# Performance work log

Measured on AMD Instinct MI355X. Metric: run time of the kernel, lower is better.

## Reference

```python
import jax, jax.numpy as jnp
import numpy as np

DIM = 256
NUM_HEADS = 4
HEAD_DIM = DIM // NUM_HEADS
EPS = 1e-5


def setup_inputs() -> dict:
    key = jax.random.key(0)
    ks = jax.random.split(key, 8)
    B, N, C = 8, 2048, DIM
    s = 0.02
    return {
        "x": jax.random.normal(ks[0], (B, N, C), jnp.float32),
        "qkv_w": jax.random.normal(ks[1], (C, 3 * C), jnp.float32) * s,
        "qkv_b": jnp.zeros((3 * C,), jnp.float32),
        "proj_w": jax.random.normal(ks[2], (C, C), jnp.float32) * s,
        "proj_b": jnp.zeros((C,), jnp.float32),
        "ln1_g": jnp.ones((C,), jnp.float32),
        "ln1_b": jnp.zeros((C,), jnp.float32),
        "ln2_g": jnp.ones((C,), jnp.float32),
        "ln2_b": jnp.zeros((C,), jnp.float32),
        "mlp_w1": jax.random.normal(ks[3], (C, 2 * C), jnp.float32) * s,
        "mlp_b1": jnp.zeros((2 * C,), jnp.float32),
        "mlp_w2": jax.random.normal(ks[4], (2 * C, C), jnp.float32) * s,
        "mlp_b2": jnp.zeros((C,), jnp.float32),
    }


def _layernorm(x, g, b):
    mu = jnp.mean(x, axis=-1, keepdims=True)
    var = jnp.mean(jnp.square(x - mu), axis=-1, keepdims=True)
    return (x - mu) * jax.lax.rsqrt(var + EPS) * g + b


def reference(x, qkv_w, qkv_b, proj_w, proj_b, ln1_g, ln1_b, ln2_g, ln2_b,
              mlp_w1, mlp_b1, mlp_w2, mlp_b2):
    B, N, C = x.shape
    H, D = NUM_HEADS, HEAD_DIM
    shortcut = x
    h = _layernorm(x, ln1_g, ln1_b)
    qkv = (h @ qkv_w + qkv_b).reshape(B, N, 3, H, D)
    q = qkv[:, :, 0].transpose(0, 2, 1, 3)  # [B,H,N,D]
    k = qkv[:, :, 1].transpose(0, 2, 1, 3)
    v = qkv[:, :, 2].transpose(0, 2, 1, 3)
    attn = jnp.einsum('bhnd,bhmd->bhnm', q, k) * (D ** -0.5)
    attn = jax.nn.softmax(attn, axis=-1)  # dropout = identity (eval mode)
    o = jnp.einsum('bhnm,bhmd->bhnd', attn, v)
    o = o.transpose(0, 2, 1, 3).reshape(B, N, C)
    x = o @ proj_w + proj_b + shortcut
    h2 = _layernorm(x, ln2_g, ln2_b)
    mlp = jax.nn.gelu(h2 @ mlp_w1 + mlp_b1, approximate=False) @ mlp_w2 + mlp_b2
    return x + mlp
```

## Files before the change

kernel.cpp:

```cpp
#include <hip/hip_runtime.h>

typedef __bf16 bf16;
typedef __bf16 bf16x8 __attribute__((ext_vector_type(8)));
typedef __bf16 bf16x4 __attribute__((ext_vector_type(4)));
typedef float  f32x4  __attribute__((ext_vector_type(4)));
typedef unsigned u32x2 __attribute__((ext_vector_type(2)));

typedef __attribute__((address_space(1))) const void GASV;
typedef __attribute__((address_space(3))) void LASV;

__device__ __forceinline__ void gload16(const void* g, void* l) {
  __builtin_amdgcn_global_load_lds((GASV*)g, (LASV*)l, 16, 0, 0);
}

constexpr float CEXP = 0.125f * 1.44269504088896340736f;

__global__ __launch_bounds__(256) void prep_fused(const float* __restrict__ qkv_w,
                                                  const float* __restrict__ proj_w,
                                                  const float* __restrict__ w1,
                                                  const float* __restrict__ w2,
                                                  bf16* __restrict__ Wtqkv,
                                                  bf16* __restrict__ WtP,
                                                  bf16* __restrict__ Wt1,
                                                  bf16* __restrict__ Wt2,
                                                  const float* __restrict__ x,
                                                  const float* __restrict__ gam,
                                                  const float* __restrict__ bet,
                                                  bf16* __restrict__ hout) {
  __shared__ float td[32][33];
  const int blk = blockIdx.x;
  const int tid = threadIdx.x;
  if (blk >= 512) {
    const int lane = tid & 63;
    const int w = tid >> 6;
    const size_t row = (size_t)(blk - 512) * 4 + w;
    const float4 v = *(const float4*)(x + row * 256 + lane * 4);
    float s1 = v.x + v.y + v.z + v.w;
    float s2 = v.x * v.x + v.y * v.y + v.z * v.z + v.w * v.w;
#pragma unroll
    for (int m = 1; m < 64; m <<= 1) {
      s1 += __shfl_xor(s1, m);
      s2 += __shfl_xor(s2, m);
    }
    const float mu = s1 * (1.0f / 256.0f);
    const float var = s2 * (1.0f / 256.0f) - mu * mu;
    const float rs = rsqrtf(var + 1e-5f);
    const float4 g4 = *(const float4*)(gam + lane * 4);
    const float4 b4 = *(const float4*)(bet + lane * 4);
    bf16x4 o;
    o[0] = (bf16)((v.x - mu) * rs * g4.x + b4.x);
    o[1] = (bf16)((v.y - mu) * rs * g4.y + b4.y);
    o[2] = (bf16)((v.z - mu) * rs * g4.z + b4.z);
    o[3] = (bf16)((v.w - mu) * rs * g4.w + b4.w);
    *(bf16x4*)(hout + row * 256 + lane * 4) = o;
    return;
  }
  const int t = blk;
  const float* src;
  bf16* dst;
  int Kin, Nin, kt, nt;
  if (t < 192)      { src = qkv_w; dst = Wtqkv; Kin = 256; Nin = 768; kt = t & 7;          nt = t >> 3; }
  else if (t < 256) { src = proj_w; dst = WtP;  Kin = 256; Nin = 256; kt = (t - 192) & 7;  nt = (t - 192) >> 3; }
  else if (t < 384) { src = w1;    dst = Wt1;   Kin = 256; Nin = 512; kt = (t - 256) & 7;  nt = (t - 256) >> 3; }
  else              { src = w2;    dst = Wt2;   Kin = 512; Nin = 256; kt = (t - 384) & 15; nt = (t - 384) >> 4; }
  {
    const int r = tid >> 3, c4 = (tid & 7) << 2;
    const float4 v = *(const float4*)(src + (size_t)(kt * 32 + r) * Nin + nt * 32 + c4);
    td[r][c4 + 0] = v.x; td[r][c4 + 1] = v.y; td[r][c4 + 2] = v.z; td[r][c4 + 3] = v.w;
  }
  __syncthreads();
  {
    const int n = tid >> 3, k4 = (tid & 7) << 2;
    bf16x4 o;
#pragma unroll
    for (int i = 0; i < 4; ++i) o[i] = (bf16)td[k4 + i][n];
    *(bf16x4*)(dst + (size_t)(nt * 32 + n) * Kin + kt * 32 + k4) = o;
  }
}

__global__ __launch_bounds__(256) void ln_fwd(const float* __restrict__ x,
                                              const float* __restrict__ gam,
                                              const float* __restrict__ bet,
                                              bf16* __restrict__ out) {
  const int lane = threadIdx.x & 63;
  const int w = threadIdx.x >> 6;
  const size_t row = (size_t)blockIdx.x * 4 + w;
  const float4 v = *(const float4*)(x + row * 256 + lane * 4);
  float s1 = v.x + v.y + v.z + v.w;
  float s2 = v.x * v.x + v.y * v.y + v.z * v.z + v.w * v.w;
#pragma unroll
  for (int m = 1; m < 64; m <<= 1) {
    s1 += __shfl_xor(s1, m);
    s2 += __shfl_xor(s2, m);
  }
  const float mu = s1 * (1.0f / 256.0f);
  const float var = s2 * (1.0f / 256.0f) - mu * mu;
  const float rs = rsqrtf(var + 1e-5f);
  const float4 g4 = *(const float4*)(gam + lane * 4);
  const float4 b4 = *(const float4*)(bet + lane * 4);
  bf16x4 o;
  o[0] = (bf16)((v.x - mu) * rs * g4.x + b4.x);
  o[1] = (bf16)((v.y - mu) * rs * g4.y + b4.y);
  o[2] = (bf16)((v.z - mu) * rs * g4.z + b4.z);
  o[3] = (bf16)((v.w - mu) * rs * g4.w + b4.w);
  *(bf16x4*)(out + row * 256 + lane * 4) = o;
}

template <int EPI, int NB>
__device__ __forceinline__ void gemm_core(bf16* __restrict__ ldsA, bf16* __restrict__ ldsB,
                                          const bf16* __restrict__ A,
                                          const bf16* __restrict__ Bt,
                                          const float* __restrict__ bias,
                                          const float* __restrict__ res,
                                          void* __restrict__ outp,
                                          int M, int N, int K, int bid) {
  const int tid = threadIdx.x;
  const int lane = tid & 63;
  const int W = tid >> 6;
  const int wm = W >> 2, wn = W & 3;
  const int qi = lane & 15, g = lane >> 4;
  const int nbm = M >> 7;
  const int bm = bid % nbm;
  const int bn = bid / nbm;
  const int m0 = bm << 7, n0 = bn << 7;
  const int nk = K >> 6;

  const char* asrc[2];
  const char* bsrc[2];
#pragma unroll
  for (int p = 0; p < 2; ++p) {
    const int s = p * 8 + W;
    const int row = (s >> 3) * 64 + ((s >> 1) & 3) * 16 + qi;
    const int kb = (s & 1) * 64 + g * 16;
    asrc[p] = (const char*)(A + (size_t)(m0 + row) * K) + kb;
    bsrc[p] = (const char*)(Bt + (size_t)(n0 + row) * K) + kb;
  }

  f32x4 acc[4][2];
#pragma unroll
  for (int i = 0; i < 4; ++i)
#pragma unroll
    for (int j = 0; j < 2; ++j) acc[i][j] = (f32x4){0.f, 0.f, 0.f, 0.f};

  auto stage = [&](int sl) {
#pragma unroll
    for (int p = 0; p < 2; ++p) {
      gload16(asrc[p], (char*)ldsA + sl * 16384 + (p * 8 + W) * 1024);
      gload16(bsrc[p], (char*)ldsB + sl * 16384 + (p * 8 + W) * 1024);
      asrc[p] += 128;
      bsrc[p] += 128;
    }
  };

  if constexpr (NB == 2) {
    stage(0);
    asm volatile("s_waitcnt vmcnt(0)" ::: "memory");
  } else {
    stage(0);
    stage(1);
    asm volatile("s_waitcnt vmcnt(4)" ::: "memory");
  }
  __builtin_amdgcn_s_barrier();

  int cur = 0, nxt = (NB == 2) ? 1 : 2;
  for (int t = 0; t < nk; ++t) {
    if constexpr (NB == 2) {
      if (t + 1 < nk) stage(nxt);
    }
    const char* pa = (const char*)ldsA + cur * 16384 + wm * 8192 + lane * 16;
    const char* pb = (const char*)ldsB + cur * 16384 + lane * 16;
    bf16x8 av[4][2], bv[2][2];
#pragma unroll
    for (int f = 0; f < 4; ++f)
#pragma unroll
      for (int ks = 0; ks < 2; ++ks)
        av[f][ks] = *(const bf16x8*)(pa + (f * 2 + ks) * 1024);
#pragma unroll
    for (int fn = 0; fn < 2; ++fn)
#pragma unroll
      for (int ks = 0; ks < 2; ++ks) {
        const int r16 = wn * 2 + fn;
        bv[fn][ks] = *(const bf16x8*)(pb + ((r16 >> 2) * 8 + (r16 & 3) * 2 + ks) * 1024);
      }
    if constexpr (NB == 3) {
      if (t + 2 < nk) stage(nxt);
    }
    __builtin_amdgcn_s_setprio(1);
#pragma unroll
    for (int fm = 0; fm < 4; ++fm)
#pragma unroll
      for (int fn = 0; fn < 2; ++fn) {
        acc[fm][fn] = __builtin_amdgcn_mfma_f32_16x16x32_bf16(av[fm][0], bv[fn][0], acc[fm][fn], 0, 0, 0);
        acc[fm][fn] = __builtin_amdgcn_mfma_f32_16x16x32_bf16(av[fm][1], bv[fn][1], acc[fm][fn], 0, 0, 0);
      }
    __builtin_amdgcn_s_setprio(0);
    if constexpr (NB == 2) {
      asm volatile("s_waitcnt vmcnt(0)" ::: "memory");
    } else {
      if (t + 2 < nk) {
        asm volatile("s_waitcnt vmcnt(4)" ::: "memory");
      } else {
        asm volatile("s_waitcnt vmcnt(0)" ::: "memory");
      }
    }
    __builtin_amdgcn_s_barrier();
    cur = (cur == NB - 1) ? 0 : cur + 1;
    nxt = (nxt == NB - 1) ? 0 : nxt + 1;
  }

#pragma unroll
  for (int fm = 0; fm < 4; ++fm)
#pragma unroll
    for (int fn = 0; fn < 2; ++fn) {
      const int r0 = m0 + wm * 64 + fm * 16 + g * 4;
      const int c = n0 + wn * 32 + fn * 16 + qi;
#pragma unroll
      for (int j = 0; j < 4; ++j) {
        const int r = r0 + j;
        const float v = acc[fm][fn][j];
        if constexpr (EPI == 0) {
          ((bf16*)outp)[(size_t)r * N + c] = (bf16)(v + bias[c]);
        } else if constexpr (EPI == 1) {
          ((bf16*)outp)[(size_t)r * 2048 + ((size_t)(c >> 11)) * 524288 + (c & 2047)] =
              (bf16)(v + bias[r]);
        } else if constexpr (EPI == 2) {
          ((float*)outp)[(size_t)r * N + c] = v + bias[c] + res[(size_t)r * N + c];
        } else {
          const float u = v + bias[c];
          ((bf16*)outp)[(size_t)r * N + c] = (bf16)(u * 0.5f * (1.0f + erff(u * 0.70710678118f)));
        }
      }
    }
}

__global__ __launch_bounds__(512) void gemm_qkv_fused(const bf16* __restrict__ h,
                                                      const bf16* __restrict__ Wtqkv,
                                                      const float* __restrict__ qkv_b,
                                                      bf16* __restrict__ qkb,
                                                      bf16* __restrict__ vT) {
  __shared__ bf16 ldsA[2 * 8192];
  __shared__ bf16 ldsB[2 * 8192];
  const int bid = (int)blockIdx.x;
  if (bid < 512) {
    gemm_core<0, 2>(ldsA, ldsB, h, Wtqkv, qkv_b, nullptr, qkb, 16384, 512, 256, bid);
  } else {
    gemm_core<1, 2>(ldsA, ldsB, Wtqkv + 512 * 256, h, qkv_b + 512, nullptr, vT,
                    256, 16384, 256, bid - 512);
  }
}

template <int EPI, int NB>
__global__ __launch_bounds__(512) void gemm_one(const bf16* __restrict__ A,
                                                const bf16* __restrict__ Bt,
                                                const float* __restrict__ bias,
                                                const float* __restrict__ res,
                                                void* __restrict__ outp,
                                                int M, int N, int K) {
  __shared__ bf16 ldsA[NB * 8192];
  __shared__ bf16 ldsB[NB * 8192];
  gemm_core<EPI, NB>(ldsA, ldsB, A, Bt, bias, res, outp, M, N, K, (int)blockIdx.x);
}

__global__ __launch_bounds__(512) void gemm_proj_merge(const bf16* __restrict__ po0,
                                                       const bf16* __restrict__ po1,
                                                       const float* __restrict__ pstats,
                                                       const bf16* __restrict__ Bt,
                                                       const float* __restrict__ bias,
                                                       const float* __restrict__ res,
                                                       float* __restrict__ outp) {
  __shared__ bf16 Al[2][8192];
  __shared__ bf16 Bl[2][8192];
  const int tid = threadIdx.x;
  const int lane = tid & 63;
  const int W = tid >> 6;
  const int wm = W >> 2, wn = W & 3;
  const int qi = lane & 15, g = lane >> 4;
  const int bm = (int)blockIdx.x & 127;
  const int bn = (int)blockIdx.x >> 7;
  const int m0 = bm << 7, n0 = bn << 7;

  int rowg[2];
  const char* asrc[2];
  const char* bsrc[2];
#pragma unroll
  for (int p = 0; p < 2; ++p) {
    const int s = p * 8 + W;
    const int row = (s >> 3) * 64 + ((s >> 1) & 3) * 16 + qi;
    const int kb = (s & 1) * 64 + g * 16;
    rowg[p] = m0 + row;
    asrc[p] = (const char*)po0 + (size_t)(m0 + row) * 512 + kb;
    bsrc[p] = (const char*)(Bt + (size_t)(n0 + row) * 256) + kb;
  }
  const size_t dpo = (size_t)((const char*)po1 - (const char*)po0);

  f32x4 acc[4][2];
#pragma unroll
  for (int i = 0; i < 4; ++i)
#pragma unroll
    for (int j = 0; j < 2; ++j) acc[i][j] = (f32x4){0.f, 0.f, 0.f, 0.f};

  bf16x8 pa0v[2], pa1v[2];
  float2 sst0[2], sst1[2];

  auto MAload = [&](int t) {
#pragma unroll
    for (int p = 0; p < 2; ++p) {
      gload16(bsrc[p], (char*)&Bl[t & 1][0] + (p * 8 + W) * 1024);
      bsrc[p] += 128;
      pa0v[p] = *(const bf16x8*)(asrc[p]);
      pa1v[p] = *(const bf16x8*)(asrc[p] + dpo);
      asrc[p] += 128;
      const int bh = ((rowg[p] >> 11) << 2) + t;
      const int ql = rowg[p] & 2047;
      sst0[p] = *(const float2*)(pstats + ((size_t)bh * 2048 + ql) * 2);
      sst1[p] = *(const float2*)(pstats + ((size_t)(bh + 32) * 2048 + ql) * 2);
    }
  };
  auto MAwrite = [&](int t) {
#pragma unroll
    for (int p = 0; p < 2; ++p) {
      const float mx = fmaxf(sst0[p].x, sst1[p].x);
      float a0 = exp2f(CEXP * (sst0[p].x - mx));
      float a1 = exp2f(CEXP * (sst1[p].x - mx));
      const float inv = 1.0f / (sst0[p].y * a0 + sst1[p].y * a1);
      a0 *= inv;
      a1 *= inv;
      bf16x8 wv;
#pragma unroll
      for (int j = 0; j < 8; ++j)
        wv[j] = (bf16)((float)pa0v[p][j] * a0 + (float)pa1v[p][j] * a1);
      *(bf16x8*)((char*)&Al[t & 1][0] + (p * 8 + W) * 1024 + lane * 16) = wv;
    }
  };

  MAload(0);
  MAwrite(0);
  asm volatile("s_waitcnt vmcnt(0) lgkmcnt(0)" ::: "memory");
  __builtin_amdgcn_s_barrier();

  for (int t = 0; t < 4; ++t) {
    if (t + 1 < 4) MAload(t + 1);
    const char* pa = (const char*)&Al[t & 1][0] + wm * 8192 + lane * 16;
    const char* pb = (const char*)&Bl[t & 1][0] + lane * 16;
    bf16x8 av[4][2], bv[2][2];
#pragma unroll
    for (int f = 0; f < 4; ++f)
#pragma unroll
      for (int ks = 0; ks < 2; ++ks)
        av[f][ks] = *(const bf16x8*)(pa + (f * 2 + ks) * 1024);
#pragma unroll
    for (int fn = 0; fn < 2; ++fn)
#pragma unroll
      for (int ks = 0; ks < 2; ++ks) {
        const int r16 = wn * 2 + fn;
        bv[fn][ks] = *(const bf16x8*)(pb + ((r16 >> 2) * 8 + (r16 & 3) * 2 + ks) * 1024);
      }
    __builtin_amdgcn_s_setprio(1);
#pragma unroll
    for (int fm = 0; fm < 4; ++fm)
#pragma unroll
      for (int fn = 0; fn < 2; ++fn) {
        acc[fm][fn] = __builtin_amdgcn_mfma_f32_16x16x32_bf16(av[fm][0], bv[fn][0], acc[fm][fn], 0, 0, 0);
        acc[fm][fn] = __builtin_amdgcn_mfma_f32_16x16x32_bf16(av[fm][1], bv[fn][1], acc[fm][fn], 0, 0, 0);
      }
    __builtin_amdgcn_s_setprio(0);
    if (t + 1 < 4) MAwrite(t + 1);
    asm volatile("s_waitcnt vmcnt(0) lgkmcnt(0)" ::: "memory");
    __builtin_amdgcn_s_barrier();
  }

#pragma unroll
  for (int fm = 0; fm < 4; ++fm)
#pragma unroll
    for (int fn = 0; fn < 2; ++fn) {
      const int r0 = m0 + wm * 64 + fm * 16 + g * 4;
      const int c = n0 + wn * 32 + fn * 16 + qi;
#pragma unroll
      for (int j = 0; j < 4; ++j) {
        const int r = r0 + j;
        outp[(size_t)r * 256 + c] = acc[fm][fn][j] + bias[c] + res[(size_t)r * 256 + c];
      }
    }
}

__global__ __launch_bounds__(256) void attn_fwd(const bf16* __restrict__ qk,
                                                const bf16* __restrict__ vT,
                                                bf16* __restrict__ po0,
                                                bf16* __restrict__ po1,
                                                float* __restrict__ pstats) {
  __shared__ bf16 Kl[3][4096];
  __shared__ bf16 Vl[2][4096];
  __shared__ bf16 Pl[4][1024];
  const int tid = threadIdx.x;
  const int lane = tid & 63;
  const int w = tid >> 6;
  const int g = lane >> 4;
  const int qi = lane & 15;
  const int bid = (int)blockIdx.x;
  const int bh = bid & 31;
  const int qt = (bid >> 5) & 15;
  const int s = bid >> 9;
  const int b = bh >> 2, h = bh & 3;

  const size_t qrow0 = (size_t)b * 2048 + qt * 128 + w * 32 + qi;
  bf16x8 qf[2][2];
#pragma unroll
  for (int f = 0; f < 2; ++f) {
    const bf16* qp = qk + (qrow0 + f * 16) * 512 + h * 64 + g * 8;
    qf[f][0] = *(const bf16x8*)qp;
    qf[f][1] = *(const bf16x8*)(qp + 32);
  }

  float mrun[2] = {0.f, 0.f};
  float lsum[2] = {0.f, 0.f};
  f32x4 o[4][2];
#pragma unroll
  for (int i = 0; i < 4; ++i)
#pragma unroll
    for (int f = 0; f < 2; ++f) o[i][f] = (f32x4){0.f, 0.f, 0.f, 0.f};

  constexpr float THR = 8.0f / CEXP;

  const char* kbase = (const char*)qk + ((size_t)b * 2048) * 1024 + 512 + h * 128 +
                      (size_t)s * 16 * 65536;
  const char* vbase = (const char*)vT + (size_t)bh * 262144 + (size_t)s * 16 * 128;
  const char* ks[2];
  const char* vs[2];
#pragma unroll
  for (int i = 0; i < 2; ++i) {
    const int fk = i * 2 + (w >> 1);
    const int half = w & 1;
    ks[i] = kbase + (fk * 16 + qi) * 1024 + half * 64 + g * 16;
    vs[i] = vbase + (size_t)(fk * 16 + qi) * 4096 + half * 64 + g * 16;
  }
  char* const pw = (char*)&Pl[w][0];
  int paddrb[2];
#pragma unroll
  for (int bb = 0; bb < 2; ++bb)
    paddrb[bb] = (bb * 2 + (g >> 1)) * 256 + qi * 16 + (g & 1) * 8;
  const char* const prd = pw + lane * 16;

  auto stageK = [&](int slot) {
    char* kd = (char*)&Kl[0][0] + slot * 8192 + w * 1024;
    gload16(ks[0], kd);
    gload16(ks[1], kd + 4096);
    ks[0] += 65536; ks[1] += 65536;
  };
  auto stageV = [&](int slot) {
    char* vd = (char*)&Vl[0][0] + slot * 8192 + w * 1024;
    gload16(vs[0], vd);
    gload16(vs[1], vd + 4096);
    vs[0] += 128; vs[1] += 128;
  };

  stageK(0);
  stageV(0);
  stageK(1);
  asm volatile("s_waitcnt vmcnt(2)" ::: "memory");
  __builtin_amdgcn_s_barrier();

  int kslot = 0, k2 = 2;
  for (int t = 0; t < 16; ++t) {
    if (t < 15) stageV((t + 1) & 1);
    if (t < 14) stageK(k2);
    const char* kb = (const char*)&Kl[0][0] + kslot * 8192 + lane * 16;
    f32x4 st[4][2];
    __builtin_amdgcn_s_setprio(1);
#pragma unroll
    for (int fk = 0; fk < 4; ++fk) {
      const bf16x8 k0 = *(const bf16x8*)(kb + fk * 2048);
      const bf16x8 k1 = *(const bf16x8*)(kb + fk * 2048 + 1024);
#pragma unroll
      for (int f = 0; f < 2; ++f) {
        f32x4 z = (f32x4){0.f, 0.f, 0.f, 0.f};
        st[fk][f] = __builtin_amdgcn_mfma_f32_16x16x32_bf16(k0, qf[f][0], z, 0, 0, 0);
        st[fk][f] = __builtin_amdgcn_mfma_f32_16x16x32_bf16(k1, qf[f][1], st[fk][f], 0, 0, 0);
      }
    }
    __builtin_amdgcn_s_setprio(0);
    float pmax[2];
#pragma unroll
    for (int f = 0; f < 2; ++f) {
      float m0 = fmaxf(fmaxf(st[0][f][0], st[0][f][1]), fmaxf(st[0][f][2], st[0][f][3]));
      float m1 = fmaxf(fmaxf(st[1][f][0], st[1][f][1]), fmaxf(st[1][f][2], st[1][f][3]));
      float m2 = fmaxf(fmaxf(st[2][f][0], st[2][f][1]), fmaxf(st[2][f][2], st[2][f][3]));
      float m3 = fmaxf(fmaxf(st[3][f][0], st[3][f][1]), fmaxf(st[3][f][2], st[3][f][3]));
      pmax[f] = fmaxf(fmaxf(m0, m1), fmaxf(m2, m3));
    }
    if (!__all(pmax[0] <= mrun[0] + THR && pmax[1] <= mrun[1] + THR)) {
#pragma unroll
      for (int f = 0; f < 2; ++f) {
        float mt = fmaxf(pmax[f], __shfl_xor(pmax[f], 16));
        mt = fmaxf(mt, __shfl_xor(mt, 32));
        const float mnew = fmaxf(mrun[f], mt);
        const float alpha = exp2f(CEXP * (mrun[f] - mnew));
        lsum[f] *= alpha;
#pragma unroll
        for (int fd = 0; fd < 4; ++fd)
#pragma unroll
          for (int j = 0; j < 4; ++j) o[fd][f][j] *= alpha;
        mrun[f] = mnew;
      }
    }
    unsigned pk[4][2][2];
#pragma unroll
    for (int f = 0; f < 2; ++f) {
      const float negcm = -CEXP * mrun[f];
      float ts = 0.f;
#pragma unroll
      for (int fk = 0; fk < 4; ++fk)
#pragma unroll
        for (int jp = 0; jp < 2; ++jp) {
          const float p0 = exp2f(fmaf(st[fk][f][2 * jp], CEXP, negcm));
          const float p1 = exp2f(fmaf(st[fk][f][2 * jp + 1], CEXP, negcm));
          ts += p0 + p1;
          union { bf16 h2[2]; unsigned u; } cv;
          cv.h2[0] = (bf16)p0;
          cv.h2[1] = (bf16)p1;
          pk[fk][f][jp] = cv.u;
        }
      lsum[f] += ts;
    }
    const char* vb = (const char*)&Vl[0][0] + (t & 1) * 8192 + lane * 16;
#pragma unroll
    for (int ksl = 0; ksl < 2; ++ksl) {
#pragma unroll
      for (int bb = 0; bb < 2; ++bb) {
        const int fk = 2 * ksl + bb;
#pragma unroll
        for (int f = 0; f < 2; ++f) {
          u32x2 pv2;
          pv2[0] = pk[fk][f][0];
          pv2[1] = pk[fk][f][1];
          *(u32x2*)(pw + f * 1024 + paddrb[bb]) = pv2;
        }
      }
      bf16x8 pa[2];
#pragma unroll
      for (int f = 0; f < 2; ++f) pa[f] = *(const bf16x8*)(prd + f * 1024);
      __builtin_amdgcn_s_setprio(1);
#pragma unroll
      for (int fd = 0; fd < 4; ++fd) {
        const bf16x8 vv = *(const bf16x8*)(vb + fd * 2048 + ksl * 1024);
#pragma unroll
        for (int f = 0; f < 2; ++f)
          o[fd][f] = __builtin_amdgcn_mfma_f32_16x16x32_bf16(vv, pa[f], o[fd][f], 0, 0, 0);
      }
      __builtin_amdgcn_s_setprio(0);
    }
    if (t < 14) {
      asm volatile("s_waitcnt vmcnt(2)" ::: "memory");
    } else {
      asm volatile("s_waitcnt vmcnt(0)" ::: "memory");
    }
    __builtin_amdgcn_s_barrier();
    kslot = (kslot == 2) ? 0 : kslot + 1;
    k2 = (k2 == 2) ? 0 : k2 + 1;
  }

#pragma unroll
  for (int f = 0; f < 2; ++f) {
    float l = lsum[f];
    l += __shfl_xor(l, 16);
    l += __shfl_xor(l, 32);
    lsum[f] = l;
  }
  if (g == 0) {
#pragma unroll
    for (int f = 0; f < 2; ++f) {
      float2 sv;
      sv.x = mrun[f];
      sv.y = lsum[f];
      *(float2*)(pstats + (((size_t)s * 32 + bh) * 2048 + qt * 128 + w * 32 + f * 16 + qi) * 2) = sv;
    }
  }
  bf16* const pob = s ? po1 : po0;
#pragma unroll
  for (int f = 0; f < 2; ++f) {
    bf16* const orow = pob + (qrow0 + f * 16) * 256 + h * 64 + g * 4;
#pragma unroll
    for (int fd = 0; fd < 4; ++fd) {
      bf16x4 ov;
#pragma unroll
      for (int j = 0; j < 4; ++j) ov[j] = (bf16)o[fd][f][j];
      *(bf16x4*)(orow + fd * 16) = ov;
    }
  }
}

extern "C" void kernel_launch(void* const* d_in, const int* in_sizes, int n_in,
                              void* d_out, int out_size, void* d_ws, size_t ws_size,
                              hipStream_t stream) {
  const float* x      = (const float*)d_in[0];
  const float* qkv_w  = (const float*)d_in[1];
  const float* qkv_b  = (const float*)d_in[2];
  const float* proj_w = (const float*)d_in[3];
  const float* proj_b = (const float*)d_in[4];
  const float* ln1_g  = (const float*)d_in[5];
  const float* ln1_b  = (const float*)d_in[6];
  const float* ln2_g  = (const float*)d_in[7];
  const float* ln2_b  = (const float*)d_in[8];
  const float* mlp_w1 = (const float*)d_in[9];
  const float* mlp_b1 = (const float*)d_in[10];
  const float* mlp_w2 = (const float*)d_in[11];
  const float* mlp_b2 = (const float*)d_in[12];
  float* out = (float*)d_out;

  char* ws = (char*)d_ws;
  bf16* Wtqkv = (bf16*)(ws);
  bf16* WtP   = (bf16*)(ws + 393216);
  bf16* Wt1   = (bf16*)(ws + 524288);
  bf16* Wt2   = (bf16*)(ws + 786432);
  bf16* h     = (bf16*)(ws + 1048576);
  bf16* qkb   = (bf16*)(ws + 9437184);
  bf16* vT    = (bf16*)(ws + 26214400);
  bf16* po1   = (bf16*)(ws + 34603008);
  float* x2   = (float*)(ws + 42991616);
  float* pstats = (float*)(ws + 59768832);
  bf16* po0 = h;
  bf16* a1 = qkb;
  bf16* h2 = h;

  prep_fused<<<4608, 256, 0, stream>>>(qkv_w, proj_w, mlp_w1, mlp_w2, Wtqkv, WtP, Wt1, Wt2,
                                       x, ln1_g, ln1_b, h);
  gemm_qkv_fused<<<768, 512, 0, stream>>>(h, Wtqkv, qkv_b, qkb, vT);
  attn_fwd<<<1024, 256, 0, stream>>>(qkb, vT, po0, po1, pstats);
  gemm_proj_merge<<<256, 512, 0, stream>>>(po0, po1, pstats, WtP, proj_b, x, x2);
  ln_fwd<<<4096, 256, 0, stream>>>(x2, ln2_g, ln2_b, h2);
  gemm_one<3, 2><<<512, 512, 0, stream>>>(h2, Wt1, mlp_b1, nullptr, a1, 16384, 512, 256);
  gemm_one<2, 3><<<256, 512, 0, stream>>>(a1, Wt2, mlp_b2, x2, out, 16384, 256, 512);
}
```

Before: 159.1 us.

## Software-pipeline attention loop so QK of next tile overlaps softmax/PV of current

Restructures the attention inner loop into a two-stage ping-pong schedule: the QK^T MFMAs for tile t+1 are issued before the softmax and PV of tile t, using two score register sets and double-buffered K/V in LDS. K buffering drops from three slots to two, and the loop is unrolled by two. The aim is to interleave exp/VALU work with matrix-core work to hide latency. In exchange it doubles the live score registers, which may hurt occupancy, and waits on vmcnt(0) at every half-step, which can expose load latency.

```diff
diff --git a/kernel.cpp b/kernel.cpp
--- a/kernel.cpp
+++ b/kernel.cpp
@@ -388,7 +388,7 @@
                                                 bf16* __restrict__ po0,
                                                 bf16* __restrict__ po1,
                                                 float* __restrict__ pstats) {
-  __shared__ bf16 Kl[3][4096];
+  __shared__ bf16 Kl[2][4096];
   __shared__ bf16 Vl[2][4096];
   __shared__ bf16 Pl[4][1024];
   const int tid = threadIdx.x;
@@ -453,18 +453,8 @@
     vs[0] += 128; vs[1] += 128;
   };
 
-  stageK(0);
-  stageV(0);
-  stageK(1);
-  asm volatile("s_waitcnt vmcnt(2)" ::: "memory");
-  __builtin_amdgcn_s_barrier();
-
-  int kslot = 0, k2 = 2;
-  for (int t = 0; t < 16; ++t) {
-    if (t < 15) stageV((t + 1) & 1);
-    if (t < 14) stageK(k2);
+  auto QK = [&](int kslot, f32x4 (&st)[4][2]) {
     const char* kb = (const char*)&Kl[0][0] + kslot * 8192 + lane * 16;
-    f32x4 st[4][2];
     __builtin_amdgcn_s_setprio(1);
 #pragma unroll
     for (int fk = 0; fk < 4; ++fk) {
@@ -478,6 +468,9 @@
       }
     }
     __builtin_amdgcn_s_setprio(0);
+  };
+
+  auto SMPV = [&](int vslot, f32x4 (&st)[4][2]) {
     float pmax[2];
 #pragma unroll
     for (int f = 0; f < 2; ++f) {
@@ -521,7 +514,7 @@
         }
       lsum[f] += ts;
     }
-    const char* vb = (const char*)&Vl[0][0] + (t & 1) * 8192 + lane * 16;
+    const char* vb = (const char*)&Vl[0][0] + vslot * 8192 + lane * 16;
 #pragma unroll
     for (int ksl = 0; ksl < 2; ++ksl) {
 #pragma unroll
@@ -548,14 +541,34 @@
       }
       __builtin_amdgcn_s_setprio(0);
     }
-    if (t < 14) {
-      asm volatile("s_waitcnt vmcnt(2)" ::: "memory");
-    } else {
-      asm volatile("s_waitcnt vmcnt(0)" ::: "memory");
-    }
+  };
+
+  f32x4 stA[4][2], stB[4][2];
+
+  stageK(0);
+  stageV(0);
+  stageK(1);
+  asm volatile("s_waitcnt vmcnt(0)" ::: "memory");
+  __builtin_amdgcn_s_barrier();
+  QK(0, stA);
+  __builtin_amdgcn_s_barrier();
+
+#pragma unroll 1
+  for (int tt = 0; tt < 8; ++tt) {
+    if (tt < 7) stageK(0);
+    stageV(1);
+    QK(1, stB);
+    SMPV(0, stA);
+    asm volatile("s_waitcnt vmcnt(0)" ::: "memory");
     __builtin_amdgcn_s_barrier();
-    kslot = (kslot == 2) ? 0 : kslot + 1;
-    k2 = (k2 == 2) ? 0 : k2 + 1;
+    if (tt < 7) {
+      stageK(1);
+      stageV(0);
+      QK(0, stA);
+    }
+    SMPV(1, stB);
+    asm volatile("s_waitcnt vmcnt(0)" ::: "memory");
+    __builtin_amdgcn_s_barrier();
   }
 
 #pragma unroll
```

Result: slower. 196.2 us (+23.3%).
